# Optimization experiments

Measured on AMD Instinct MI355X. Metric: run time of the kernel, lower is better.

The kernel has to match this reference:

```python
import jax, jax.numpy as jnp
import numpy as np

N, E, H, DIN, NL = 16384, 524288, 128, 1024, 3
H4 = 4 * H
EPS = 1e-7  # GENConv message eps


def _ln(x, g, b, eps=1e-5):
    mu = jnp.mean(x, axis=-1, keepdims=True)
    var = jnp.var(x, axis=-1, keepdims=True)
    return (x - mu) * jax.lax.rsqrt(var + eps) * g + b


def _genconv(x, src, dst, ew, w1, b1, lng, lnb, w2, b2, t):
    # message: relu(x_j + edge_weight) + eps  -> [E, H]
    msg = jax.nn.relu(x[src] + ew[:, None]) + EPS
    # softmax aggregation with learnable temperature t over incoming edges
    logit = msg * t
    m = jax.ops.segment_max(logit, dst, num_segments=N)
    m = jnp.where(jnp.isfinite(m), m, 0.0)
    e = jnp.exp(logit - m[dst])
    denom = jax.ops.segment_sum(e, dst, num_segments=N)
    alpha = e / (denom[dst] + 1e-16)
    agg = jax.ops.segment_sum(msg * alpha, dst, num_segments=N)  # [N, H]
    h = agg + x  # GENConv adds root features before MLP
    # MLP: Linear(H,2H) -> LayerNorm -> ReLU -> Linear(2H,H)
    return jax.nn.relu(_ln(h @ w1 + b1, lng, lnb)) @ w2 + b2


def _forward(edge_index, features, edge_weight, fc_w, fc_b, conv_w1, conv_b1,
             conv_lng, conv_lnb, conv_w2, conv_b2, conv_t, blk_lng, blk_lnb,
             phi_w, phi_b, attn_wa, attn_ba, attn_wb, attn_bb, attn_wc, attn_bc,
             rho_w, rho_b, clf_w, clf_b):
    src, dst = edge_index[0], edge_index[1]
    x = jax.nn.relu(features @ fc_w + fc_b)  # [N, H]
    x_ = x
    # layers[0]: conv only (no norm/act/residual)
    x = _genconv(x, src, dst, edge_weight, conv_w1[0], conv_b1[0], conv_lng[0],
                 conv_lnb[0], conv_w2[0], conv_b2[0], conv_t[0])
    x_ = jnp.concatenate([x_, x], axis=1)
    # layers[1:]: DeepGCNLayer block='res': x + relu(LN(conv(x))) (eval: dropout=id)
    for i in (1, 2):
        h = _genconv(x, src, dst, edge_weight, conv_w1[i], conv_b1[i], conv_lng[i],
                     conv_lnb[i], conv_w2[i], conv_b2[i], conv_t[i])
        h = jax.nn.relu(_ln(h, blk_lng[i], blk_lnb[i]))
        x = x + h
        x_ = jnp.concatenate([x_, x], axis=1)
    # x_: [N, 4H]
    hp = jax.nn.relu(x_ @ phi_w + phi_b)
    a = jnp.tanh(hp @ attn_wa + attn_ba)
    b = jax.nn.sigmoid(hp @ attn_wb + attn_bb)
    A = (a * b) @ attn_wc + attn_bc  # [N, 1]
    w = jax.nn.softmax(A[:, 0])      # softmax over nodes
    pooled = w @ hp                  # [4H]
    out = jax.nn.relu(pooled @ rho_w + rho_b)
    return out @ clf_w + clf_b       # [num_classes]


def setup_inputs() -> dict:
    key = jax.random.key(0)
    ks = jax.random.split(key, 16)
    sc = 0.05
    rn = lambda k, shp: jax.random.normal(k, shp, jnp.float32) * sc
    return {
        "features": jax.random.normal(ks[0], (N, DIN), jnp.float32),
        "edge_index": jax.random.randint(ks[1], (2, E), 0, N),
        "edge_weight": jax.random.uniform(ks[2], (E,), jnp.float32),
        "fc_w": rn(ks[3], (DIN, H)), "fc_b": jnp.zeros((H,), jnp.float32),
        "conv_w1": rn(ks[4], (NL, H, 2 * H)), "conv_b1": jnp.zeros((NL, 2 * H), jnp.float32),
        "conv_lng": jnp.ones((NL, 2 * H), jnp.float32), "conv_lnb": jnp.zeros((NL, 2 * H), jnp.float32),
        "conv_w2": rn(ks[5], (NL, 2 * H, H)), "conv_b2": jnp.zeros((NL, H), jnp.float32),
        "conv_t": jnp.ones((NL,), jnp.float32),
        "blk_lng": jnp.ones((NL, H), jnp.float32), "blk_lnb": jnp.zeros((NL, H), jnp.float32),
        "phi_w": rn(ks[6], (H4, H4)), "phi_b": jnp.zeros((H4,), jnp.float32),
        "attn_wa": rn(ks[7], (H4, H4)), "attn_ba": jnp.zeros((H4,), jnp.float32),
        "attn_wb": rn(ks[8], (H4, H4)), "attn_bb": jnp.zeros((H4,), jnp.float32),
        "attn_wc": rn(ks[9], (H4, 1)), "attn_bc": jnp.zeros((1,), jnp.float32),
        "rho_w": rn(ks[10], (H4, H4)), "rho_b": jnp.zeros((H4,), jnp.float32),
        "clf_w": rn(ks[11], (H4, 3)), "clf_b": jnp.zeros((3,), jnp.float32),
    }


def reference(features, edge_index, edge_weight, fc_w, fc_b, conv_w1, conv_b1,
              conv_lng, conv_lnb, conv_w2, conv_b2, conv_t, blk_lng, blk_lnb,
              phi_w, phi_b, attn_wa, attn_ba, attn_wb, attn_bb, attn_wc, attn_bc,
              rho_w, rho_b, clf_w, clf_b):
    return _forward(edge_index, features, edge_weight, fc_w, fc_b, conv_w1, conv_b1,
                    conv_lng, conv_lnb, conv_w2, conv_b2, conv_t, blk_lng, blk_lnb,
                    phi_w, phi_b, attn_wa, attn_ba, attn_wb, attn_bb, attn_wc,
                    attn_bc, rho_w, rho_b, clf_w, clf_b)
```

## Files before the change

### kernel.cpp

```cpp
#include <hip/hip_runtime.h>
#include <hip/hip_bf16.h>
#include <cstdint>
#include <cstddef>

#define N_NODES 16384
#define N_EDGES 524288

using bf16 = __hip_bfloat16;
typedef short bf16x8 __attribute__((ext_vector_type(8)));
typedef float f32x4 __attribute__((ext_vector_type(4)));

__device__ __forceinline__ float bf2f(bf16 v) { return __bfloat162float(v); }
__device__ __forceinline__ float ldv(const void* p, size_t i, int f32) {
    return f32 ? ((const float*)p)[i] : bf2f(((const bf16*)p)[i]);
}
__device__ __forceinline__ float us2f(unsigned short u) {
    unsigned int x = ((unsigned int)u) << 16;
    return __uint_as_float(x);
}
__device__ __forceinline__ unsigned short f2us(float f) {
    bf16 b = __float2bfloat16(f);
    return *(unsigned short*)&b;
}
__device__ __forceinline__ float ftanh(float v) { return 1.f - 2.f / (__expf(2.f * v) + 1.f); }
__device__ __forceinline__ float fsig(float v)  { return 1.f / (1.f + __expf(-v)); }

__global__ void zero_k(const unsigned int* __restrict__ lng, int* __restrict__ dtf,
                       uint4* __restrict__ base, int n16) {
    if (blockIdx.x == 0 && threadIdx.x == 0)
        dtf[0] = (lng[0] == 0x3F800000u) ? 1 : 0;
    uint4 z = {0, 0, 0, 0};
    for (int i = blockIdx.x * blockDim.x + threadIdx.x; i < n16; i += gridDim.x * blockDim.x)
        base[i] = z;
}

#define NSEG 10
struct TranspDesc {
    const void* W[NSEG];
    bf16* WT[NSEG];
    int woff[NSEG];
    int N[NSEG];
    int ostride[NSEG];
    int tstart[NSEG + 1];
};

__global__ __launch_bounds__(256) void transp_all_k(TranspDesc d, const int* __restrict__ dtf) {
    __shared__ float tile[32][33];
    int f32 = dtf[0];
    int b = blockIdx.x;
    int s = 0;
    #pragma unroll
    for (int j = 1; j < NSEG; j++) if (b >= d.tstart[j]) s = j;
    int tloc = b - d.tstart[s];
    int N = d.N[s];
    int tpn = N >> 5;
    int tk = tloc / tpn, tn = tloc - tk * tpn;
    int k0 = tk * 32, n0 = tn * 32;
    int t = threadIdx.x;
    int c = t & 31, r0 = t >> 5;
    #pragma unroll
    for (int j = 0; j < 4; j++) {
        int r = r0 + 8 * j;
        tile[r][c] = ldv(d.W[s], (size_t)d.woff[s] + (size_t)(k0 + r) * N + n0 + c, f32);
    }
    __syncthreads();
    bf16* wt = d.WT[s];
    int ost = d.ostride[s];
    #pragma unroll
    for (int j = 0; j < 4; j++) {
        int r = r0 + 8 * j;
        wt[(size_t)(n0 + r) * ost + k0 + c] = __float2bfloat16(tile[c][r]);
    }
}

#define GLD(gp, lp) __builtin_amdgcn_global_load_lds( \
    (const __attribute__((address_space(1))) void*)(gp), \
    (__attribute__((address_space(3))) void*)(lp), 16, 0, 0)

template <int ACT, int PIPE, int MR>
__global__ __launch_bounds__(256) void mgemm_k(
    const bf16* __restrict__ A, const bf16* __restrict__ Aalt, int sel, int lda,
    const bf16* __restrict__ WT,
    const void* __restrict__ bias, const void* __restrict__ bias2, size_t boff,
    bf16* __restrict__ C, int ldc, int K, const int* __restrict__ dtf,
    const void* __restrict__ aux1, const void* __restrict__ aux2, size_t aoff,
    const bf16* __restrict__ xold, bf16* __restrict__ xnew,
    float* __restrict__ Aout)
{
    constexpr int NI  = MR / 32;
    constexpr int NP  = MR / 16;
    constexpr int TSZ = MR * 32 + 128 * 32;
    constexpr int LREQ = (PIPE ? 2 * TSZ : TSZ);
    constexpr int LBUF = (MR * 128 > LREQ) ? MR * 128 : LREQ;
    __shared__ unsigned short lbuf[LBUF];
    __shared__ float wcs[64];
    const int f32 = dtf[0];
    const bf16* Ap = (sel && f32) ? Aalt : A;
    int tid = threadIdx.x;
    int wave = tid >> 6, lane = tid & 63;
    int row0 = blockIdx.x * MR, col0 = blockIdx.y * 128;
    const bf16* Ag = Ap + (size_t)row0 * lda;
    const bf16* Bg = WT + (size_t)col0 * K;

    f32x4 acc[NI][4] = {};
    int fr = lane & 15, fg = lane >> 4;
    int wr = (wave >> 1) * (MR / 2), wc = (wave & 1) * 64;
    int rchunk = fg ^ ((fr >> 1) & 3);

    if (ACT == 4 && tid < 64) wcs[tid] = ldv(aux1, (size_t)(col0 >> 1) + tid, f32);

    if constexpr (PIPE == 0) {
        static_assert(MR == 128, "PIPE=0 path hardcodes 128-row geometry");
        unsigned short* lA0 = lbuf;
        unsigned short* lA1 = lbuf + 4096;
        unsigned short* lB0 = lbuf + 8192;
        unsigned short* lB1 = lbuf + 12288;
        for (int k0 = 0; k0 < K; k0 += 64) {
            #pragma unroll
            for (int j = 0; j < 2; j++) {
                int li = j * 256 + tid;
                int r = li >> 2, kc = li & 3;
                int kcs = kc ^ ((r >> 1) & 3);
                char* dA = (char*)lA0 + j * 4096 + wave * 1024;
                char* dB = (char*)lB0 + j * 4096 + wave * 1024;
                GLD(Ag + (size_t)r * lda + k0 + kcs * 8, dA);
                GLD(Bg + (size_t)r * K   + k0 + kcs * 8, dB);
            }
            #pragma unroll
            for (int j = 0; j < 2; j++) {
                int li = j * 256 + tid;
                int r = li >> 2, kc = li & 3;
                int kcs = kc ^ ((r >> 1) & 3);
                char* dA = (char*)lA1 + j * 4096 + wave * 1024;
                char* dB = (char*)lB1 + j * 4096 + wave * 1024;
                GLD(Ag + (size_t)r * lda + k0 + 32 + kcs * 8, dA);
                GLD(Bg + (size_t)r * K   + k0 + 32 + kcs * 8, dB);
            }
            __syncthreads();
            {
                bf16x8 aF[4], bF[4];
                #pragma unroll
                for (int i = 0; i < 4; i++) {
                    aF[i] = *(const bf16x8*)&lA0[(wr + i * 16 + fr) * 32 + rchunk * 8];
                    bF[i] = *(const bf16x8*)&lB0[(wc + i * 16 + fr) * 32 + rchunk * 8];
                }
                #pragma unroll
                for (int i = 0; i < 4; i++)
                    #pragma unroll
                    for (int j = 0; j < 4; j++)
                        acc[i][j] = __builtin_amdgcn_mfma_f32_16x16x32_bf16(aF[i], bF[j], acc[i][j], 0, 0, 0);
            }
            {
                bf16x8 aF[4], bF[4];
                #pragma unroll
                for (int i = 0; i < 4; i++) {
                    aF[i] = *(const bf16x8*)&lA1[(wr + i * 16 + fr) * 32 + rchunk * 8];
                    bF[i] = *(const bf16x8*)&lB1[(wc + i * 16 + fr) * 32 + rchunk * 8];
                }
                #pragma unroll
                for (int i = 0; i < 4; i++)
                    #pragma unroll
                    for (int j = 0; j < 4; j++)
                        acc[i][j] = __builtin_amdgcn_mfma_f32_16x16x32_bf16(aF[i], bF[j], acc[i][j], 0, 0, 0);
            }
            __syncthreads();
        }
    } else {
        auto stage = [&](unsigned short* dst, int k0) {
            #pragma unroll
            for (int j = 0; j < MR / 64; j++) {
                int li = j * 256 + tid;
                int r = li >> 2, kc = li & 3;
                int kcs = kc ^ ((r >> 1) & 3);
                GLD(Ag + (size_t)r * lda + k0 + kcs * 8, (char*)dst + li * 16);
            }
            #pragma unroll
            for (int j = 0; j < 2; j++) {
                int li = j * 256 + tid;
                int r = li >> 2, kc = li & 3;
                int kcs = kc ^ ((r >> 1) & 3);
                GLD(Bg + (size_t)r * K + k0 + kcs * 8, (char*)(dst + MR * 32) + li * 16);
            }
        };
        auto compute = [&](const unsigned short* sA) {
            const unsigned short* sB = sA + MR * 32;
            bf16x8 aF[NI], bF[4];
            #pragma unroll
            for (int i = 0; i < NI; i++)
                aF[i] = *(const bf16x8*)&sA[(wr + i * 16 + fr) * 32 + rchunk * 8];
            #pragma unroll
            for (int j = 0; j < 4; j++)
                bF[j] = *(const bf16x8*)&sB[(wc + j * 16 + fr) * 32 + rchunk * 8];
            #pragma unroll
            for (int i = 0; i < NI; i++)
                #pragma unroll
                for (int j = 0; j < 4; j++)
                    acc[i][j] = __builtin_amdgcn_mfma_f32_16x16x32_bf16(aF[i], bF[j], acc[i][j], 0, 0, 0);
        };

        stage(lbuf, 0);
        int bsel = 0;
        for (int k0 = 0; k0 < K; k0 += 32) {
            __syncthreads();
            if (k0 + 32 < K) stage(lbuf + (bsel ^ 1) * TSZ, k0 + 32);
            compute(lbuf + bsel * TSZ);
            bsel ^= 1;
        }
        __syncthreads();
    }

    unsigned short* lC = lbuf;
    #pragma unroll
    for (int j = 0; j < 4; j++) {
        int col = wc + j * 16 + fr;
        float bv;
        if (ACT == 4) {
            int pair = (col0 + col) >> 1;
            bv = (fr & 1) ? ldv(bias2, pair, f32) : ldv(bias, pair, f32);
        } else {
            bv = ldv(bias, boff + col0 + col, f32);
        }
        #pragma unroll
        for (int i = 0; i < NI; i++) {
            #pragma unroll
            for (int rr = 0; rr < 4; rr++) {
                int row = wr + i * 16 + fg * 4 + rr;
                float v = acc[i][j][rr] + bv;
                if (ACT == 1) v = fmaxf(v, 0.f);
                else if (ACT == 2) v = ftanh(v);
                else if (ACT == 3) v = fsig(v);
                else if (ACT == 4) v = (fr & 1) ? fsig(v) : ftanh(v);
                int scol = col ^ ((row & 3) << 5);
                lC[row * 128 + scol] = f2us(v);
            }
        }
    }
    __syncthreads();

    if (ACT == 4) {
        int p0 = (tid & 15) * 4;
        #pragma unroll
        for (int pass = 0; pass < NP; pass++) {
            int r = pass * 16 + (tid >> 4);
            int sc = ((tid & 15) * 8) ^ ((r & 3) << 5);
            unsigned short v[8];
            *(uint4*)v = *(const uint4*)&lC[r * 128 + sc];
            float s = us2f(v[0]) * us2f(v[1]) * wcs[p0]
                    + us2f(v[2]) * us2f(v[3]) * wcs[p0 + 1]
                    + us2f(v[4]) * us2f(v[5]) * wcs[p0 + 2]
                    + us2f(v[6]) * us2f(v[7]) * wcs[p0 + 3];
            #pragma unroll
            for (int m = 1; m < 16; m <<= 1) s += __shfl_xor(s, m, 64);
            if ((tid & 15) == 0) atomicAdd(&Aout[row0 + r], s);
        }
        return;
    }

    if (ACT == 5) {
        int cl = (tid & 15) * 8;
        float gr[8], brr[8];
        #pragma unroll
        for (int k = 0; k < 8; k++) {
            gr[k]  = ldv(aux1, aoff + cl + k, f32);
            brr[k] = ldv(aux2, aoff + cl + k, f32);
        }
        #pragma unroll
        for (int pass = 0; pass < NP; pass++) {
            int r = pass * 16 + (tid >> 4);
            int sc = cl ^ ((r & 3) << 5);
            unsigned short v[8];
            *(uint4*)v = *(const uint4*)&lC[r * 128 + sc];
            float x[8], s = 0.f;
            #pragma unroll
            for (int k = 0; k < 8; k++) { x[k] = us2f(v[k]); s += x[k]; }
            #pragma unroll
            for (int m = 1; m < 16; m <<= 1) s += __shfl_xor(s, m, 64);
            float mu = s * (1.f / 128.f);
            float q = 0.f;
            #pragma unroll
            for (int k = 0; k < 8; k++) { x[k] -= mu; q += x[k] * x[k]; }
            #pragma unroll
            for (int m = 1; m < 16; m <<= 1) q += __shfl_xor(q, m, 64);
            float rstd = rsqrtf(q * (1.f / 128.f) + 1e-5f);
            unsigned short xo[8], o[8];
            *(uint4*)xo = *(const uint4*)(xold + (size_t)(row0 + r) * 512 + cl);
            #pragma unroll
            for (int k = 0; k < 8; k++) {
                float y = fmaxf(x[k] * rstd * gr[k] + brr[k], 0.f);
                o[k] = f2us(us2f(xo[k]) + y);
            }
            *(uint4*)(xnew + (size_t)(row0 + r) * 512 + cl) = *(const uint4*)o;
        }
        return;
    }

    #pragma unroll
    for (int pass = 0; pass < NP; pass++) {
        int r = pass * 16 + (tid >> 4);
        int c = (tid & 15) * 8;
        int sc = c ^ ((r & 3) << 5);
        *(uint4*)(C + (size_t)(row0 + r) * ldc + col0 + c) = *(const uint4*)&lC[r * 128 + sc];
    }
}

static void* const force_inst_mgemm_ab = (void*)mgemm_k<4, 0, 128>;

__global__ __launch_bounds__(256) void abgemm_k(
    const bf16* __restrict__ A, int lda,
    const bf16* __restrict__ WT,
    const void* __restrict__ bias, const void* __restrict__ bias2,
    int K, const int* __restrict__ dtf,
    const void* __restrict__ aux1,
    float* __restrict__ Aout)
{
    __shared__ unsigned short lbuf[12288];
    __shared__ float wcs[64];
    const int f32 = dtf[0];
    int tid = threadIdx.x;
    int wave = tid >> 6, lane = tid & 63;
    int row0 = blockIdx.x * 64, col0 = blockIdx.y * 128;
    const bf16* Ag = A + (size_t)row0 * lda;
    const bf16* Bg = WT + (size_t)col0 * K;

    f32x4 acc[2][4] = {};
    int fr = lane & 15, fg = lane >> 4;
    int wr = (wave >> 1) * 32, wc = (wave & 1) * 64;
    int rchunk = fg ^ ((fr >> 1) & 3);

    if (tid < 64) wcs[tid] = ldv(aux1, (size_t)(col0 >> 1) + tid, f32);

    unsigned short* lA0 = lbuf;
    unsigned short* lA1 = lbuf + 2048;
    unsigned short* lB0 = lbuf + 4096;
    unsigned short* lB1 = lbuf + 8192;
    for (int k0 = 0; k0 < K; k0 += 64) {
        {
            int r = tid >> 2, kc = tid & 3;
            int kcs = kc ^ ((r >> 1) & 3);
            GLD(Ag + (size_t)r * lda + k0 + kcs * 8,      (char*)lA0 + tid * 16);
            GLD(Ag + (size_t)r * lda + k0 + 32 + kcs * 8, (char*)lA1 + tid * 16);
        }
        #pragma unroll
        for (int j = 0; j < 2; j++) {
            int li = j * 256 + tid;
            int r = li >> 2, kc = li & 3;
            int kcs = kc ^ ((r >> 1) & 3);
            GLD(Bg + (size_t)r * K + k0 + kcs * 8,      (char*)lB0 + li * 16);
            GLD(Bg + (size_t)r * K + k0 + 32 + kcs * 8, (char*)lB1 + li * 16);
        }
        __syncthreads();
        {
            bf16x8 aF[2], bF[4];
            #pragma unroll
            for (int i = 0; i < 2; i++)
                aF[i] = *(const bf16x8*)&lA0[(wr + i * 16 + fr) * 32 + rchunk * 8];
            #pragma unroll
            for (int j = 0; j < 4; j++)
                bF[j] = *(const bf16x8*)&lB0[(wc + j * 16 + fr) * 32 + rchunk * 8];
            #pragma unroll
            for (int i = 0; i < 2; i++)
                #pragma unroll
                for (int j = 0; j < 4; j++)
                    acc[i][j] = __builtin_amdgcn_mfma_f32_16x16x32_bf16(aF[i], bF[j], acc[i][j], 0, 0, 0);
        }
        {
            bf16x8 aF[2], bF[4];
            #pragma unroll
            for (int i = 0; i < 2; i++)
                aF[i] = *(const bf16x8*)&lA1[(wr + i * 16 + fr) * 32 + rchunk * 8];
            #pragma unroll
            for (int j = 0; j < 4; j++)
                bF[j] = *(const bf16x8*)&lB1[(wc + j * 16 + fr) * 32 + rchunk * 8];
            #pragma unroll
            for (int i = 0; i < 2; i++)
                #pragma unroll
                for (int j = 0; j < 4; j++)
                    acc[i][j] = __builtin_amdgcn_mfma_f32_16x16x32_bf16(aF[i], bF[j], acc[i][j], 0, 0, 0);
        }
        __syncthreads();
    }

    unsigned short* lC = lbuf;
    #pragma unroll
    for (int j = 0; j < 4; j++) {
        int col = wc + j * 16 + fr;
        int pair = (col0 + col) >> 1;
        float bv = (fr & 1) ? ldv(bias2, pair, f32) : ldv(bias, pair, f32);
        #pragma unroll
        for (int i = 0; i < 2; i++) {
            #pragma unroll
            for (int rr = 0; rr < 4; rr++) {
                int row = wr + i * 16 + fg * 4 + rr;
                float v = acc[i][j][rr] + bv;
                v = (fr & 1) ? fsig(v) : ftanh(v);
                int scol = col ^ ((row & 3) << 5);
                lC[row * 128 + scol] = f2us(v);
            }
        }
    }
    __syncthreads();

    int p0 = (tid & 15) * 4;
    #pragma unroll
    for (int pass = 0; pass < 4; pass++) {
        int r = pass * 16 + (tid >> 4);
        int sc = ((tid & 15) * 8) ^ ((r & 3) << 5);
        unsigned short v[8];
        *(uint4*)v = *(const uint4*)&lC[r * 128 + sc];
        float s = us2f(v[0]) * us2f(v[1]) * wcs[p0]
                + us2f(v[2]) * us2f(v[3]) * wcs[p0 + 1]
                + us2f(v[4]) * us2f(v[5]) * wcs[p0 + 2]
                + us2f(v[6]) * us2f(v[7]) * wcs[p0 + 3];
        #pragma unroll
        for (int m = 1; m < 16; m <<= 1) s += __shfl_xor(s, m, 64);
        if ((tid & 15) == 0) atomicAdd(&Aout[row0 + r], s);
    }
}

__global__ __launch_bounds__(256) void fcgemm_k(
    const float* __restrict__ Af, const bf16* __restrict__ Ab,
    const bf16* __restrict__ WT,
    const void* __restrict__ bias,
    bf16* __restrict__ C, int ldc, const int* __restrict__ dtf)
{
    constexpr int K = 1024;
    constexpr int TSZ = 64 * 32 + 128 * 32;
    __shared__ unsigned short lbuf[2 * TSZ];
    const int f32 = dtf[0];
    int tid = threadIdx.x;
    int wave = tid >> 6, lane = tid & 63;
    int fr = lane & 15, fg = lane >> 4;
    int wr = (wave >> 1) * 32, wc = (wave & 1) * 64;
    int rchunk = fg ^ ((fr >> 1) & 3);
    int row0 = blockIdx.x * 64;
    const float* Agf = Af + (size_t)row0 * K;
    const bf16*  Agb = Ab + (size_t)row0 * K;
    const bf16* Bg = WT;

    f32x4 acc[2][4] = {};

    auto stage = [&](unsigned short* dst, int k0) {
        {
            int r = tid >> 2, kc = tid & 3;
            int kcs = kc ^ ((r >> 1) & 3);
            if (f32) {
                const float* src = Agf + (size_t)r * K + k0 + kcs * 8;
                float4 v0 = *(const float4*)src;
                float4 v1 = *(const float4*)(src + 4);
                unsigned short o[8];
                o[0] = f2us(v0.x); o[1] = f2us(v0.y); o[2] = f2us(v0.z); o[3] = f2us(v0.w);
                o[4] = f2us(v1.x); o[5] = f2us(v1.y); o[6] = f2us(v1.z); o[7] = f2us(v1.w);
                *(uint4*)((char*)dst + tid * 16) = *(const uint4*)o;
            } else {
                GLD(Agb + (size_t)r * K + k0 + kcs * 8, (char*)dst + tid * 16);
            }
        }
        #pragma unroll
        for (int j = 0; j < 2; j++) {
            int li = j * 256 + tid;
            int r = li >> 2, kc = li & 3;
            int kcs = kc ^ ((r >> 1) & 3);
            GLD(Bg + (size_t)r * K + k0 + kcs * 8, (char*)(dst + 64 * 32) + li * 16);
        }
    };

    stage(lbuf, 0);
    int bsel = 0;
    for (int k0 = 0; k0 < K; k0 += 32) {
        __syncthreads();
        if (k0 + 32 < K) stage(lbuf + (bsel ^ 1) * TSZ, k0 + 32);
        const unsigned short* sA = lbuf + bsel * TSZ;
        const unsigned short* sB = sA + 64 * 32;
        bf16x8 aF[2], bF[4];
        #pragma unroll
        for (int i = 0; i < 2; i++)
            aF[i] = *(const bf16x8*)&sA[(wr + i * 16 + fr) * 32 + rchunk * 8];
        #pragma unroll
        for (int j = 0; j < 4; j++)
            bF[j] = *(const bf16x8*)&sB[(wc + j * 16 + fr) * 32 + rchunk * 8];
        #pragma unroll
        for (int i = 0; i < 2; i++)
            #pragma unroll
            for (int j = 0; j < 4; j++)
                acc[i][j] = __builtin_amdgcn_mfma_f32_16x16x32_bf16(aF[i], bF[j], acc[i][j], 0, 0, 0);
        bsel ^= 1;
    }
    __syncthreads();

    unsigned short* lC = lbuf;
    #pragma unroll
    for (int j = 0; j < 4; j++) {
        int col = wc + j * 16 + fr;
        float bv = ldv(bias, col, f32);
        #pragma unroll
        for (int i = 0; i < 2; i++) {
            #pragma unroll
            for (int rr = 0; rr < 4; rr++) {
                int row = wr + i * 16 + fg * 4 + rr;
                float v = fmaxf(acc[i][j][rr] + bv, 0.f);
                int scol = col ^ ((row & 3) << 5);
                lC[row * 128 + scol] = f2us(v);
            }
        }
    }
    __syncthreads();
    #pragma unroll
    for (int pass = 0; pass < 4; pass++) {
        int r = pass * 16 + (tid >> 4);
        int c = (tid & 15) * 8;
        int sc = c ^ ((r & 3) << 5);
        *(uint4*)(C + (size_t)(row0 + r) * ldc + c) = *(const uint4*)&lC[r * 128 + sc];
    }
}

__global__ __launch_bounds__(256) void c1ln_k(
    const bf16* __restrict__ A, const bf16* __restrict__ WT,
    const void* __restrict__ bias, size_t boff,
    const void* __restrict__ g, const void* __restrict__ b, size_t goff,
    const int* __restrict__ dtf, bf16* __restrict__ out)
{
    constexpr int K = 128;
    constexpr int TSZ = 64 * 32 + 256 * 32;
    __shared__ unsigned short lbuf[2 * TSZ];
    const int f32 = dtf[0];
    int tid = threadIdx.x;
    int wave = tid >> 6, lane = tid & 63;
    int fr = lane & 15, fg = lane >> 4;
    int rchunk = fg ^ ((fr >> 1) & 3);
    int row0 = blockIdx.x * 64;
    const bf16* Ag = A + (size_t)row0 * K;
    const bf16* Bg = WT;

    f32x4 acc[16] = {};

    auto stage = [&](unsigned short* dst, int k0) {
        {
            int r = tid >> 2, kc = tid & 3;
            int kcs = kc ^ ((r >> 1) & 3);
            GLD(Ag + (size_t)r * K + k0 + kcs * 8, (char*)dst + tid * 16);
        }
        #pragma unroll
        for (int j = 0; j < 4; j++) {
            int li = j * 256 + tid;
            int r = li >> 2, kc = li & 3;
            int kcs = kc ^ ((r >> 1) & 3);
            GLD(Bg + (size_t)r * K + k0 + kcs * 8, (char*)(dst + 64 * 32) + li * 16);
        }
    };

    stage(lbuf, 0);
    int bsel = 0;
    for (int k0 = 0; k0 < K; k0 += 32) {
        __syncthreads();
        if (k0 + 32 < K) stage(lbuf + (bsel ^ 1) * TSZ, k0 + 32);
        const unsigned short* sA = lbuf + bsel * TSZ;
        const unsigned short* sB = sA + 64 * 32;
        bf16x8 aF = *(const bf16x8*)&sA[(wave * 16 + fr) * 32 + rchunk * 8];
        #pragma unroll
        for (int j = 0; j < 16; j++) {
            bf16x8 bF = *(const bf16x8*)&sB[(j * 16 + fr) * 32 + rchunk * 8];
            acc[j] = __builtin_amdgcn_mfma_f32_16x16x32_bf16(aF, bF, acc[j], 0, 0, 0);
        }
        bsel ^= 1;
    }
    __syncthreads();

    float bv[16], gv[16], bb[16];
    #pragma unroll
    for (int j = 0; j < 16; j++) {
        int col = j * 16 + fr;
        bv[j] = ldv(bias, boff + col, f32);
        gv[j] = ldv(g, goff + col, f32);
        bb[j] = ldv(b, goff + col, f32);
    }
    unsigned short* lC = lbuf;
    #pragma unroll
    for (int rr = 0; rr < 4; rr++) {
        int row = wave * 16 + fg * 4 + rr;
        float v[16], s = 0.f;
        #pragma unroll
        for (int j = 0; j < 16; j++) { v[j] = acc[j][rr] + bv[j]; s += v[j]; }
        #pragma unroll
        for (int m = 1; m < 16; m <<= 1) s += __shfl_xor(s, m, 64);
        float mu = s * (1.f / 256.f);
        float q = 0.f;
        #pragma unroll
        for (int j = 0; j < 16; j++) { v[j] -= mu; q += v[j] * v[j]; }
        #pragma unroll
        for (int m = 1; m < 16; m <<= 1) q += __shfl_xor(q, m, 64);
        float rstd = rsqrtf(q * (1.f / 256.f) + 1e-5f);
        int swz = ((row >> 2) & 3) << 4;
        #pragma unroll
        for (int j = 0; j < 16; j++) {
            int col = j * 16 + fr;
            float y = fmaxf(v[j] * rstd * gv[j] + bb[j], 0.f);
            lC[row * 256 + (col ^ swz)] = f2us(y);
        }
    }
    __syncthreads();
    #pragma unroll
    for (int pass = 0; pass < 8; pass++) {
        int r = pass * 8 + (tid >> 5);
        int c = (tid & 31) * 8;
        int sc = c ^ (((r >> 2) & 3) << 4);
        *(uint4*)(out + (size_t)(row0 + r) * 256 + c) = *(const uint4*)&lC[r * 256 + sc];
    }
}

__global__ void hist_k(const int* __restrict__ dst, int* __restrict__ deg, int E) {
    int e = blockIdx.x * blockDim.x + threadIdx.x;
    if (e < E) atomicAdd(&deg[dst[e]], 1);
}

__global__ __launch_bounds__(1024) void scan_k(const int* __restrict__ deg,
                                               int* __restrict__ offs,
                                               int* __restrict__ cursor, int n) {
    __shared__ int part[1024];
    int tid = threadIdx.x;
    int base = tid * 16;
    int local[16];
    int s = 0;
    #pragma unroll
    for (int i = 0; i < 16; i++) { local[i] = deg[base + i]; s += local[i]; }
    part[tid] = s;
    __syncthreads();
    for (int o = 1; o < 1024; o <<= 1) {
        int v = (tid >= o) ? part[tid - o] : 0;
        __syncthreads();
        part[tid] += v;
        __syncthreads();
    }
    int run = part[tid] - s;
    #pragma unroll
    for (int i = 0; i < 16; i++) {
        offs[base + i] = run;
        cursor[base + i] = run;
        run += local[i];
    }
    if (tid == 1023) offs[n] = run;
}

__global__ void scatter_k(const int* __restrict__ src, const int* __restrict__ dst,
                          const void* __restrict__ ew, const int* __restrict__ dtf,
                          int* __restrict__ cursor, int2* __restrict__ csr_pack, int E) {
    int e = blockIdx.x * blockDim.x + threadIdx.x;
    if (e < E) {
        int f32 = dtf[0];
        int d = dst[e];
        int p = atomicAdd(&cursor[d], 1);
        int2 rec;
        rec.x = src[e];
        rec.y = __float_as_int(ldv(ew, e, f32));
        csr_pack[p] = rec;
    }
}

__global__ __launch_bounds__(256) void agg_k(
    const bf16* __restrict__ xin, int ldx,
    const int* __restrict__ offs, const int2* __restrict__ csr_pack,
    const void* __restrict__ conv_t, int layer, const int* __restrict__ dtf,
    bf16* __restrict__ hout)
{
    __shared__ float red[4][32][9];
    int node = blockIdx.x;
    int tid = threadIdx.x;
    int wv = tid >> 6, lane = tid & 63;
    int hl = lane >> 5, ll = lane & 31;
    int f32 = dtf[0];
    float t = ldv(conv_t, layer, f32);
    int s0 = offs[node], s1 = offs[node + 1];
    float ss0 = 0.f, ss1 = 0.f, ss2 = 0.f, ss3 = 0.f;
    float ws0 = 0.f, ws1 = 0.f, ws2 = 0.f, ws3 = 0.f;
    const bf16* xcol = xin + ll * 4;

    auto body = [&](uint2 xv, float ewv) {
        float x0 = us2f((unsigned short)xv.x);
        float x1 = us2f((unsigned short)(xv.x >> 16));
        float x2 = us2f((unsigned short)xv.y);
        float x3 = us2f((unsigned short)(xv.y >> 16));
        float m0 = fmaxf(x0 + ewv, 0.f) + 1e-7f;
        float m1 = fmaxf(x1 + ewv, 0.f) + 1e-7f;
        float m2 = fmaxf(x2 + ewv, 0.f) + 1e-7f;
        float m3 = fmaxf(x3 + ewv, 0.f) + 1e-7f;
        float e0 = __expf(fminf(m0 * t, 80.f));
        float e1 = __expf(fminf(m1 * t, 80.f));
        float e2 = __expf(fminf(m2 * t, 80.f));
        float e3 = __expf(fminf(m3 * t, 80.f));
        ss0 += e0; ws0 += m0 * e0;
        ss1 += e1; ws1 += m1 * e1;
        ss2 += e2; ws2 += m2 * e2;
        ss3 += e3; ws3 += m3 * e3;
    };

    int p = s0 + wv * 2 + hl;
    for (; p + 8 < s1; p += 16) {
        int2 rA = csr_pack[p];
        int2 rB = csr_pack[p + 8];
        uint2 xa = *(const uint2*)(xcol + (size_t)rA.x * ldx);
        uint2 xb = *(const uint2*)(xcol + (size_t)rB.x * ldx);
        body(xa, __int_as_float(rA.y));
        body(xb, __int_as_float(rB.y));
    }
    if (p < s1) {
        int2 rA = csr_pack[p];
        uint2 xa = *(const uint2*)(xcol + (size_t)rA.x * ldx);
        body(xa, __int_as_float(rA.y));
    }

    ss0 += __shfl_xor(ss0, 32, 64); ws0 += __shfl_xor(ws0, 32, 64);
    ss1 += __shfl_xor(ss1, 32, 64); ws1 += __shfl_xor(ws1, 32, 64);
    ss2 += __shfl_xor(ss2, 32, 64); ws2 += __shfl_xor(ws2, 32, 64);
    ss3 += __shfl_xor(ss3, 32, 64); ws3 += __shfl_xor(ws3, 32, 64);
    if (hl == 0) {
        red[wv][ll][0] = ss0; red[wv][ll][1] = ss1;
        red[wv][ll][2] = ss2; red[wv][ll][3] = ss3;
        red[wv][ll][4] = ws0; red[wv][ll][5] = ws1;
        red[wv][ll][6] = ws2; red[wv][ll][7] = ws3;
    }
    __syncthreads();
    if (tid < 32) {
        float S0 = 0, S1 = 0, S2 = 0, S3 = 0, W0 = 0, W1 = 0, W2 = 0, W3 = 0;
        #pragma unroll
        for (int w = 0; w < 4; w++) {
            S0 += red[w][tid][0]; S1 += red[w][tid][1];
            S2 += red[w][tid][2]; S3 += red[w][tid][3];
            W0 += red[w][tid][4]; W1 += red[w][tid][5];
            W2 += red[w][tid][6]; W3 += red[w][tid][7];
        }
        uint2 sv = *(const uint2*)(xin + (size_t)node * ldx + tid * 4);
        float o0 = W0 / (S0 + 1e-16f) + us2f((unsigned short)sv.x);
        float o1 = W1 / (S1 + 1e-16f) + us2f((unsigned short)(sv.x >> 16));
        float o2 = W2 / (S2 + 1e-16f) + us2f((unsigned short)sv.y);
        float o3 = W3 / (S3 + 1e-16f) + us2f((unsigned short)(sv.y >> 16));
        uint2 ov;
        ov.x = (unsigned int)f2us(o0) | ((unsigned int)f2us(o1) << 16);
        ov.y = (unsigned int)f2us(o2) | ((unsigned int)f2us(o3) << 16);
        *(uint2*)(hout + (size_t)node * 128 + tid * 4) = ov;
    }
}

__global__ __launch_bounds__(256) void pooled_k(const float* __restrict__ A,
                                                const bf16* __restrict__ hp,
                                                float* __restrict__ pooled,
                                                float* __restrict__ sumexp,
                                                int rowsPerBlk) {
    int tid = threadIdx.x;
    int r0 = blockIdx.x * rowsPerBlk;
    float a0 = 0.f, a1 = 0.f, se = 0.f;
    for (int r = 0; r < rowsPerBlk; r++) {
        int n = r0 + r;
        float wn = __expf(A[n]);
        se += wn;
        const bf16* hr = hp + (size_t)n * 512;
        a0 += wn * bf2f(hr[tid]);
        a1 += wn * bf2f(hr[tid + 256]);
    }
    atomicAdd(&pooled[tid], a0);
    atomicAdd(&pooled[tid + 256], a1);
    if (tid == 0) atomicAdd(sumexp, se);
}

__global__ __launch_bounds__(256) void rho_part_k(
    const float* __restrict__ pooled,
    const void* __restrict__ rw,
    const int* __restrict__ dtf,
    float* __restrict__ vacc) {
    int col = blockIdx.x * 256 + threadIdx.x;
    int k0 = blockIdx.y * 16;
    int f32 = dtf[0];
    float acc = 0.f;
    #pragma unroll
    for (int i = 0; i < 16; i++)
        acc = fmaf(pooled[k0 + i], ldv(rw, (size_t)(k0 + i) * 512 + col, f32), acc);
    atomicAdd(&vacc[col], acc);
}

__global__ __launch_bounds__(64) void clf_k(const float* __restrict__ vacc,
                                            const float* __restrict__ sumexp,
                                            const void* __restrict__ rb,
                                            const void* __restrict__ cw,
                                            const void* __restrict__ cb,
                                            const int* __restrict__ dtf,
                                            void* __restrict__ out) {
    int lane = threadIdx.x;
    int f32 = dtf[0];
    float inv = 1.f / (*sumexp);
    #pragma unroll
    for (int t = 0; t < 3; t++) {
        float acc = 0.f;
        for (int j = lane; j < 512; j += 64) {
            float vj = fmaxf(vacc[j] * inv + ldv(rb, j, f32), 0.f);
            acc += vj * ldv(cw, (size_t)j * 3 + t, f32);
        }
        for (int s = 32; s > 0; s >>= 1) acc += __shfl_xor(acc, s, 64);
        if (lane == 0) {
            float o = acc + ldv(cb, t, f32);
            if (f32) ((float*)out)[t] = o;
            else     ((bf16*)out)[t] = __float2bfloat16(o);
        }
    }
}

extern "C" void kernel_launch(void* const* d_in, const int* in_sizes, int n_in,
                              void* d_out, int out_size, void* d_ws, size_t ws_size,
                              hipStream_t stream) {
    const void* features = d_in[0];
    const int*  eidx     = (const int*)d_in[1];
    const void* ew       = d_in[2];
    const void* fc_w     = d_in[3];
    const void* fc_b     = d_in[4];
    const void* conv_w1  = d_in[5];
    const void* conv_b1  = d_in[6];
    const void* conv_lng = d_in[7];
    const void* conv_lnb = d_in[8];
    const void* conv_w2  = d_in[9];
    const void* conv_b2  = d_in[10];
    const void* conv_t   = d_in[11];
    const void* blk_lng  = d_in[12];
    const void* blk_lnb  = d_in[13];
    const void* phi_w    = d_in[14];
    const void* phi_b    = d_in[15];
    const void* attn_wa  = d_in[16];
    const void* attn_ba  = d_in[17];
    const void* attn_wb  = d_in[18];
    const void* attn_bb  = d_in[19];
    const void* attn_wc  = d_in[20];
    const void* rho_w    = d_in[22];
    const void* rho_b    = d_in[23];
    const void* clf_w    = d_in[24];
    const void* clf_b    = d_in[25];

    const int* src = eidx;
    const int* dst = eidx + N_EDGES;

    char* wsp = (char*)d_ws;
    size_t off = 0;
    auto alloc = [&](size_t bytes) -> void* {
        void* p = wsp + off;
        off = (off + bytes + 255) & ~(size_t)255;
        return p;
    };
    int*   dtf    = (int*)alloc(256);
    float* sumexp = (float*)alloc(256);
    float* vec    = (float*)alloc(512 * 4);
    float* pooled = (float*)alloc(512 * 4);
    int*   deg    = (int*)alloc((size_t)N_NODES * 4);
    int*   offs   = (int*)alloc((size_t)(N_NODES + 1) * 4);
    int*   cursor = (int*)alloc((size_t)N_NODES * 4);
    float* Aw     = (float*)alloc((size_t)N_NODES * 4);
    int2*  csr_pack = (int2*)alloc((size_t)N_EDGES * 8);
    bf16* WT_fc  = (bf16*)alloc((size_t)128 * 1024 * 2);
    bf16* WT_c1  = (bf16*)alloc((size_t)3 * 256 * 128 * 2);
    bf16* WT_c2  = (bf16*)alloc((size_t)3 * 128 * 256 * 2);
    bf16* WT_phi = (bf16*)alloc((size_t)512 * 512 * 2);
    bf16* WT_ab  = (bf16*)alloc((size_t)1024 * 512 * 2);
    bf16* x_cat   = (bf16*)alloc((size_t)N_NODES * 512 * 2);
    bf16* scratch = (bf16*)alloc((size_t)N_NODES * 512 * 2);
    bf16* hp      = (bf16*)alloc((size_t)N_NODES * 512 * 2);

    bf16* h_tmp  = scratch;
    bf16* mid    = scratch + (size_t)N_NODES * 128;

    size_t zbytes = (size_t)((char*)(Aw + N_NODES) - (char*)sumexp);
    zero_k<<<64, 256, 0, stream>>>((const unsigned int*)conv_lng, dtf,
                                   (uint4*)sumexp, (int)(zbytes / 16));

    TranspDesc td{};
    int pos = 0, si = 0;
    auto seg = [&](const void* W, int woff, bf16* WT, int K, int N, int ostride) {
        td.W[si] = W; td.woff[si] = woff; td.WT[si] = WT;
        td.N[si] = N; td.ostride[si] = ostride; td.tstart[si] = pos;
        pos += (K / 32) * (N / 32); si++;
    };
    seg(fc_w, 0, WT_fc, 1024, 128, 1024);
    for (int l = 0; l < 3; l++) seg(conv_w1, l * 128 * 256, WT_c1 + (size_t)l * 256 * 128, 128, 256, 128);
    for (int l = 0; l < 3; l++) seg(conv_w2, l * 256 * 128, WT_c2 + (size_t)l * 128 * 256, 256, 128, 256);
    seg(phi_w, 0, WT_phi, 512, 512, 512);
    seg(attn_wa, 0, WT_ab, 512, 512, 1024);
    seg(attn_wb, 0, WT_ab + 512, 512, 512, 1024);
    td.tstart[NSEG] = pos;
    transp_all_k<<<pos, 256, 0, stream>>>(td, dtf);

    hist_k<<<N_EDGES / 256, 256, 0, stream>>>(dst, deg, N_EDGES);
    scan_k<<<1, 1024, 0, stream>>>(deg, offs, cursor, N_NODES);
    scatter_k<<<N_EDGES / 256, 256, 0, stream>>>(src, dst, ew, dtf, cursor, csr_pack, N_EDGES);

    fcgemm_k<<<256, 256, 0, stream>>>(
        (const float*)features, (const bf16*)features, WT_fc, fc_b,
        x_cat, 512, dtf);

    for (int l = 0; l < 3; l++) {
        const bf16* x_in = x_cat + (size_t)l * 128;
        agg_k<<<N_NODES, 256, 0, stream>>>(x_in, 512, offs, csr_pack, conv_t, l, dtf, h_tmp);
        c1ln_k<<<256, 256, 0, stream>>>(
            h_tmp, WT_c1 + (size_t)l * 256 * 128,
            conv_b1, (size_t)l * 256, conv_lng, conv_lnb, (size_t)l * 256,
            dtf, mid);
        if (l == 0) {
            mgemm_k<0, 1, 64><<<dim3(256, 1), 256, 0, stream>>>(
                mid, mid, 0, 256, WT_c2 + (size_t)l * 128 * 256,
                conv_b2, conv_b2, (size_t)l * 128, x_cat + 128, 512, 256, dtf,
                nullptr, nullptr, 0, nullptr, nullptr, nullptr);
        } else {
            mgemm_k<5, 1, 64><<<dim3(256, 1), 256, 0, stream>>>(
                mid, mid, 0, 256, WT_c2 + (size_t)l * 128 * 256,
                conv_b2, conv_b2, (size_t)l * 128, hp , 512, 256, dtf,
                blk_lng, blk_lnb, (size_t)l * 128,
                x_cat + (size_t)l * 128, x_cat + (size_t)(l + 1) * 128, nullptr);
        }
    }

    mgemm_k<1, 1, 64><<<dim3(256, 4), 256, 0, stream>>>(
        x_cat, x_cat, 0, 512, WT_phi, phi_b, phi_b, 0, hp, 512, 512, dtf,
        nullptr, nullptr, 0, nullptr, nullptr, nullptr);
    abgemm_k<<<dim3(256, 8), 256, 0, stream>>>(
        hp, 512, WT_ab, attn_ba, attn_bb, 512, dtf, attn_wc, Aw);
    pooled_k<<<256, 256, 0, stream>>>(Aw, hp, pooled, sumexp, N_NODES / 256);
    rho_part_k<<<dim3(2, 32), 256, 0, stream>>>(pooled, rho_w, dtf, vec);
    clf_k<<<1, 64, 0, stream>>>(vec, sumexp, rho_b, clf_w, clf_b, dtf, d_out);
}
```

Measured before the change: 468.1 us.

## Replace global-atomic CSR scatter with two-pass bucketed binning

Builds the CSR edge list in two passes. The first pass bins edges into 256 coarse destination buckets using shared-memory histograms and one global atomic per bucket per block. The second pass places each bucket's edges into final CSR positions using per-node LDS atomics. This removes per-edge global atomics and scattered 8-byte writes, at the cost of an extra kernel and intermediate buffer. It assumes each bucket holds at most 3072 edges and that source indices fit in 14 bits, so skewed degree distributions could overflow a bucket.

```diff
diff --git a/kernel.cpp b/kernel.cpp
--- a/kernel.cpp
+++ b/kernel.cpp
@@ -652,6 +652,62 @@
         rec.x = src[e];
         rec.y = __float_as_int(ldv(ew, e, f32));
         csr_pack[p] = rec;
+    }
+}
+
+#define BCAP 3072
+
+__global__ __launch_bounds__(256) void bin_k(
+    const int* __restrict__ src, const int* __restrict__ dst,
+    const void* __restrict__ ew, const int* __restrict__ dtf,
+    int* __restrict__ bcursor, int2* __restrict__ bucketArr) {
+    __shared__ int hist[256];
+    __shared__ int base[256];
+    int tid = threadIdx.x;
+    int e0 = blockIdx.x * 2048;
+    int f32 = dtf[0];
+    hist[tid] = 0;
+    __syncthreads();
+    int d[8];
+    #pragma unroll
+    for (int i = 0; i < 8; i++) {
+        d[i] = dst[e0 + i * 256 + tid];
+        atomicAdd(&hist[d[i] >> 6], 1);
+    }
+    __syncthreads();
+    base[tid] = atomicAdd(&bcursor[tid], hist[tid]);
+    __syncthreads();
+    hist[tid] = 0;
+    __syncthreads();
+    #pragma unroll
+    for (int i = 0; i < 8; i++) {
+        int e = e0 + i * 256 + tid;
+        int b = d[i] >> 6;
+        int rank = atomicAdd(&hist[b], 1);
+        int2 rec;
+        rec.x = src[e] | ((d[i] & 63) << 14);
+        rec.y = __float_as_int(ldv(ew, e, f32));
+        bucketArr[(size_t)b * BCAP + base[b] + rank] = rec;
+    }
+}
+
+__global__ __launch_bounds__(256) void debin_k(
+    const int2* __restrict__ bucketArr, const int* __restrict__ bcursor,
+    const int* __restrict__ offs, int2* __restrict__ csr_pack) {
+    __shared__ int lcur[64];
+    __shared__ int lbase[64];
+    int tid = threadIdx.x;
+    int b = blockIdx.x;
+    if (tid < 64) { lcur[tid] = 0; lbase[tid] = offs[b * 64 + tid]; }
+    __syncthreads();
+    int cnt = bcursor[b];
+    for (int i = tid; i < cnt; i += 256) {
+        int2 rec = bucketArr[(size_t)b * BCAP + i];
+        int dlow = rec.x >> 14;
+        int s = rec.x & 16383;
+        int rank = atomicAdd(&lcur[dlow], 1);
+        int2 o; o.x = s; o.y = rec.y;
+        csr_pack[lbase[dlow] + rank] = o;
     }
 }
 
@@ -848,7 +904,9 @@
     int*   offs   = (int*)alloc((size_t)(N_NODES + 1) * 4);
     int*   cursor = (int*)alloc((size_t)N_NODES * 4);
     float* Aw     = (float*)alloc((size_t)N_NODES * 4);
+    int*   bcursor = (int*)alloc(256 * 4);
     int2*  csr_pack = (int2*)alloc((size_t)N_EDGES * 8);
+    int2*  bucketArr = (int2*)alloc((size_t)256 * BCAP * 8);
     bf16* WT_fc  = (bf16*)alloc((size_t)128 * 1024 * 2);
     bf16* WT_c1  = (bf16*)alloc((size_t)3 * 256 * 128 * 2);
     bf16* WT_c2  = (bf16*)alloc((size_t)3 * 128 * 256 * 2);
@@ -861,7 +919,7 @@
     bf16* h_tmp  = scratch;
     bf16* mid    = scratch + (size_t)N_NODES * 128;
 
-    size_t zbytes = (size_t)((char*)(Aw + N_NODES) - (char*)sumexp);
+    size_t zbytes = (size_t)((char*)bcursor + 1024 - (char*)sumexp);
     zero_k<<<64, 256, 0, stream>>>((const unsigned int*)conv_lng, dtf,
                                    (uint4*)sumexp, (int)(zbytes / 16));
 
@@ -883,7 +941,8 @@
 
     hist_k<<<N_EDGES / 256, 256, 0, stream>>>(dst, deg, N_EDGES);
     scan_k<<<1, 1024, 0, stream>>>(deg, offs, cursor, N_NODES);
-    scatter_k<<<N_EDGES / 256, 256, 0, stream>>>(src, dst, ew, dtf, cursor, csr_pack, N_EDGES);
+    bin_k<<<256, 256, 0, stream>>>(src, dst, ew, dtf, bcursor, bucketArr);
+    debin_k<<<256, 256, 0, stream>>>(bucketArr, bcursor, offs, csr_pack);
 
     fcgemm_k<<<256, 256, 0, stream>>>(
         (const float*)features, (const bf16*)features, WT_fc, fc_b,
```

After: 452.1 us. 3.4% less time.
